# Performance work log

Measured on AMD Instinct MI355X. Metric: run time of the kernel, lower is better.

Reference implementation:

```python
import jax, jax.numpy as jnp
import numpy as np

B, S, D, U = 4, 2048, 1024, 1024

def setup_inputs() -> dict:
    key = jax.random.key(0)
    k0, k1, k2, k3 = jax.random.split(key, 4)
    scale = 1.0 / np.sqrt(D)  # keep logits sane; Glorot-like magnitude
    return {
        "inputs": jax.random.normal(k0, (B, S, D), dtype=jnp.float32),
        "W_q": jax.random.normal(k1, (D, U), dtype=jnp.float32) * scale,
        "W_k": jax.random.normal(k2, (D, U), dtype=jnp.float32) * scale,
        "W_v": jax.random.normal(k3, (D, U), dtype=jnp.float32) * scale,
    }

def reference(inputs, W_q, W_k, W_v):
    # QKV projections: [B,S,D] @ [D,U] -> [B,S,U]
    q = jnp.einsum("bsd,du->bsu", inputs, W_q)
    k = jnp.einsum("bsd,du->bsu", inputs, W_k)
    v = jnp.einsum("bsd,du->bsu", inputs, W_v)
    # Unscaled attention, as in the source (no 1/sqrt(d) factor)
    scores = jnp.einsum("bqu,bku->bqk", q, k)          # [B,S,S]
    weights = jax.nn.softmax(scores, axis=-1)
    return jnp.einsum("bqk,bku->bqu", weights, v)       # [B,S,U]
```

## Files before the change

### kernel.cpp

```cpp
#include <hip/hip_runtime.h>
#include <cstdint>
#include <cstddef>


typedef unsigned short ushort_t;
typedef _Float16 half_t;
typedef __attribute__((ext_vector_type(8))) short short8;
typedef __attribute__((ext_vector_type(4))) float floatx4;

__device__ inline unsigned short h2u(half_t h) {
  union { half_t h; unsigned short u; } v; v.h = h; return v.u;
}

__device__ __forceinline__ void gload16(const half_t* g, half_t* l) {
  __builtin_amdgcn_global_load_lds(
      (const __attribute__((address_space(1))) unsigned int*)g,
      (__attribute__((address_space(3))) unsigned int*)l, 16, 0, 0);
}

#define MX 8192
#define KCAT 2048

#define XCAT_OFF 0UL
#define WT_OFF   50331648UL
#define S_OFF    0UL
#define QCAT_OFF 69206016UL
#define KCAT_OFF 119537664UL
#define VT_OFF   169869312UL
#define WS_NEED  186646528UL

__global__ __launch_bounds__(256) void k_split_x(const float* __restrict__ X,
                                                 half_t* __restrict__ xcat) {
  long long i = (long long)blockIdx.x * 256 + threadIdx.x;
  float x = X[i];
  half_t h = (half_t)x;
  half_t lo = (half_t)(x - (float)h);
  long long row = i >> 10;
  int col = (int)(i & 1023);
  half_t* r = xcat + row * KCAT;
  r[col] = h;
  r[col + 1024] = lo;
}

__global__ __launch_bounds__(256) void k_split_wt(const float* __restrict__ Wq,
                                                  const float* __restrict__ Wk,
                                                  const float* __restrict__ Wv,
                                                  half_t* __restrict__ wt) {
  __shared__ float tile[64][65];
  const float* W = (blockIdx.z == 0) ? Wq : ((blockIdx.z == 1) ? Wk : Wv);
  half_t* out = wt + (size_t)blockIdx.z * 1024 * KCAT;
  int d0 = blockIdx.y * 64, u0 = blockIdx.x * 64;
  int t = threadIdx.x;
  int tr = t >> 6, tc = t & 63;
  for (int r = 0; r < 64; r += 4)
    tile[r + tr][tc] = W[(size_t)(d0 + r + tr) * 1024 + (u0 + tc)];
  __syncthreads();
  for (int r = 0; r < 64; r += 4) {
    int urow = r + tr, dcol = tc;
    float x = tile[dcol][urow];
    half_t h = (half_t)x;
    half_t* o = out + (size_t)(u0 + urow) * KCAT + d0;
    o[dcol] = h;
    o[dcol + 1024] = h;
  }
}

enum { EP_F32 = 0, EP_QK = 1, EP_VT = 2 };

template <int MODE>
__global__ __launch_bounds__(256, 4) void k_gemm(
    const half_t* __restrict__ A, long long aBatch, int lda,
    const half_t* __restrict__ Bt, long long bBatch, int ldb,
    void* __restrict__ Cout, long long cBatch, int ldc, int K,
    half_t* __restrict__ CoutK) {
  __shared__ __align__(16) half_t As[128 * 64];
  __shared__ __align__(16) half_t Bs[128 * 64];
  const int t = threadIdx.x;
  const int z = blockIdx.z;
  A += (long long)z * aBatch;
  Bt += (long long)z * bBatch;
  const int m0 = blockIdx.y * 128, n0 = blockIdx.x * 128;

  const int w = t >> 6, l = t & 63;
  const int lr = l & 15, quad = l >> 4;
  const int wm = (w >> 1) * 64, wn = (w & 1) * 64;

  const floatx4 fz = {0.f, 0.f, 0.f, 0.f};
  floatx4 acc[4][4];
#pragma unroll
  for (int i = 0; i < 4; i++)
#pragma unroll
    for (int j = 0; j < 4; j++) acc[i][j] = fz;

  const half_t* Ap[4];
  const half_t* Bp[4];
  half_t* ldsA[4];
  half_t* ldsB[4];
#pragma unroll
  for (int s = 0; s < 4; s++) {
    int c = s * 256 + t;
    int row = c >> 3, gq = (c & 7) ^ ((c >> 3) & 7);
    Ap[s] = A + (long long)(m0 + row) * lda + gq * 8;
    Bp[s] = Bt + (long long)(n0 + row) * ldb + gq * 8;
    ldsA[s] = &As[(s * 256 + w * 64) * 8];
    ldsB[s] = &Bs[(s * 256 + w * 64) * 8];
  }

  const int p0 = quad ^ (lr & 7);
  const int p1 = (quad + 4) ^ (lr & 7);
  const int arow = (wm + lr) * 64, brow = (wn + lr) * 64;

  for (int kb = 0; kb < K; kb += 64) {
    __syncthreads();
#pragma unroll
    for (int s = 0; s < 4; s++) {
      gload16(Ap[s] + kb, ldsA[s]);
      gload16(Bp[s] + kb, ldsB[s]);
    }
    __syncthreads();
#pragma unroll
    for (int s = 0; s < 2; s++) {
      const int pp = s ? p1 : p0;
      short8 af[4], bfg[4];
#pragma unroll
      for (int j = 0; j < 4; j++) bfg[j] = *(const short8*)&Bs[brow + j * 1024 + pp * 8];
#pragma unroll
      for (int i = 0; i < 4; i++) af[i] = *(const short8*)&As[arow + i * 1024 + pp * 8];
#pragma unroll
      for (int i = 0; i < 4; i++)
#pragma unroll
        for (int j = 0; j < 4; j++)
          acc[i][j] = __builtin_amdgcn_mfma_f32_16x16x32_f16(af[i], bfg[j], acc[i][j], 0, 0, 0);
    }
  }

#pragma unroll
  for (int i = 0; i < 4; i++) {
#pragma unroll
    for (int j = 0; j < 4; j++) {
#pragma unroll
      for (int r = 0; r < 4; r++) {
        int grow = m0 + wm + i * 16 + quad * 4 + r;
        int gcol = n0 + wn + j * 16 + lr;
        float v = acc[i][j][r];
        if (MODE == EP_F32) {
          float* C = (float*)Cout + (long long)z * cBatch;
          C[(long long)grow * ldc + gcol] = v;
        } else if (MODE == EP_QK) {
          int sel = gcol >> 10;
          int ucol = gcol & 1023;
          half_t h = (half_t)v;
          if (sel == 0) {
            half_t* pq = (half_t*)Cout + (long long)grow * KCAT;
            pq[ucol] = h;
            pq[ucol + 1024] = (half_t)(v - (float)h);
          } else {
            half_t* pk = CoutK + (long long)grow * KCAT;
            pk[ucol] = h;
            pk[ucol + 1024] = h;
          }
        } else {
          half_t* C = (half_t*)Cout;
          int b = grow >> 11, s = grow & 2047;
          C[((long long)b * 1024 + gcol) * 2048 + s] = (half_t)v;
        }
      }
    }
  }
}

__global__ __launch_bounds__(256) void k_softmax(float* __restrict__ Sbuf) {
  long long row = blockIdx.x;
  float* p = Sbuf + row * 2048;
  int t = threadIdx.x;
  float4 v0 = ((const float4*)p)[t];
  float4 v1 = ((const float4*)p)[t + 256];
  float m = fmaxf(fmaxf(fmaxf(v0.x, v0.y), fmaxf(v0.z, v0.w)),
                  fmaxf(fmaxf(v1.x, v1.y), fmaxf(v1.z, v1.w)));
  for (int off = 32; off; off >>= 1) m = fmaxf(m, __shfl_xor(m, off));
  __shared__ float red[8];
  int wv = t >> 6, ln = t & 63;
  if (ln == 0) red[wv] = m;
  __syncthreads();
  m = fmaxf(fmaxf(red[0], red[1]), fmaxf(red[2], red[3]));
  float e0 = __expf(v0.x - m), e1 = __expf(v0.y - m), e2 = __expf(v0.z - m), e3 = __expf(v0.w - m);
  float e4 = __expf(v1.x - m), e5 = __expf(v1.y - m), e6 = __expf(v1.z - m), e7 = __expf(v1.w - m);
  float s = ((e0 + e1) + (e2 + e3)) + ((e4 + e5) + (e6 + e7));
  for (int off = 32; off; off >>= 1) s += __shfl_xor(s, off);
  if (ln == 0) red[4 + wv] = s;
  __syncthreads();
  s = (red[4] + red[5]) + (red[6] + red[7]);
  float inv = 1.0f / s;
  uint2 w0, w1;
  w0.x = (unsigned)h2u((half_t)(e0 * inv)) | ((unsigned)h2u((half_t)(e1 * inv)) << 16);
  w0.y = (unsigned)h2u((half_t)(e2 * inv)) | ((unsigned)h2u((half_t)(e3 * inv)) << 16);
  w1.x = (unsigned)h2u((half_t)(e4 * inv)) | ((unsigned)h2u((half_t)(e5 * inv)) << 16);
  w1.y = (unsigned)h2u((half_t)(e6 * inv)) | ((unsigned)h2u((half_t)(e7 * inv)) << 16);
  ((uint2*)p)[t] = w0;
  ((uint2*)p)[t + 256] = w1;
}

extern "C" void kernel_launch(void* const* d_in, const int* in_sizes, int n_in,
                              void* d_out, int out_size, void* d_ws, size_t ws_size,
                              hipStream_t stream) {
  (void)in_sizes; (void)n_in; (void)out_size;
  if (ws_size < WS_NEED) return;

  const float* X = (const float*)d_in[0];
  const float* Wq = (const float*)d_in[1];
  const float* Wk = (const float*)d_in[2];
  const float* Wv = (const float*)d_in[3];
  char* ws = (char*)d_ws;
  half_t* xcat = (half_t*)(ws + XCAT_OFF);
  half_t* wt = (half_t*)(ws + WT_OFF);
  float* Sbuf = (float*)(ws + S_OFF);
  half_t* qcat = (half_t*)(ws + QCAT_OFF);
  half_t* kcat = (half_t*)(ws + KCAT_OFF);
  half_t* vt = (half_t*)(ws + VT_OFF);
  float* out = (float*)d_out;

  k_split_x<<<dim3(MX * 1024 / 256), dim3(256), 0, stream>>>(X, xcat);
  k_split_wt<<<dim3(16, 16, 3), dim3(256), 0, stream>>>(Wq, Wk, Wv, wt);

  k_gemm<EP_QK><<<dim3(16, 64, 1), dim3(256), 0, stream>>>(
      xcat, 0LL, KCAT, wt, 0LL, KCAT, qcat, 0LL, 0, KCAT, kcat);

  k_gemm<EP_VT><<<dim3(8, 64, 1), dim3(256), 0, stream>>>(
      xcat, 0LL, KCAT, wt + 2 * 1024 * KCAT, 0LL, KCAT, vt, 0LL, 0, 1024, nullptr);

  k_gemm<EP_F32><<<dim3(16, 16, 4), dim3(256), 0, stream>>>(
      qcat, (long long)2048 * KCAT, KCAT, kcat, (long long)2048 * KCAT, KCAT,
      Sbuf, (long long)2048 * 2048, 2048, KCAT, nullptr);

  k_softmax<<<dim3(8192), dim3(256), 0, stream>>>(Sbuf);

  k_gemm<EP_F32><<<dim3(8, 16, 4), dim3(256), 0, stream>>>(
      (const half_t*)Sbuf, (long long)2048 * 4096, 4096,
      vt, (long long)1024 * 2048, 2048,
      out, (long long)2048 * 1024, 1024, 2048, nullptr);
}
```

Before: 347.6 us.

## Add 256x256-tile double-buffered GEMM for QK projection and score GEMMs

Adds a new 512-thread GEMM kernel with 256x256 output tiles, a double-buffered LDS pipeline split into half-K stages, explicit vmcnt/lgkmcnt waits and raw barriers, and MFMA priority raising. It replaces the 128x128 GEMM for the fused Q/K projection and the QK^T score GEMM. The aim is to overlap global-to-LDS loads with MFMA work and to raise arithmetic intensity per tile. The cost is 128KB of LDS and heavy register use per block, and fewer blocks in flight (256 for both GEMMs).

```diff
diff --git a/kernel.cpp b/kernel.cpp
--- a/kernel.cpp
+++ b/kernel.cpp
@@ -17,6 +17,11 @@
       (const __attribute__((address_space(1))) unsigned int*)g,
       (__attribute__((address_space(3))) unsigned int*)l, 16, 0, 0);
 }
+
+#define BAR() asm volatile("s_barrier" ::: "memory")
+#define LGKM0() asm volatile("s_waitcnt lgkmcnt(0)" ::: "memory")
+#define VM6() asm volatile("s_waitcnt vmcnt(6)" ::: "memory")
+#define VM0() asm volatile("s_waitcnt vmcnt(0)" ::: "memory")
 
 #define MX 8192
 #define KCAT 2048
@@ -167,6 +172,147 @@
       }
     }
   }
+}
+
+template <int MODE>
+__global__ __launch_bounds__(512, 2) void k_gemm256(
+    const half_t* __restrict__ A, long long aBatch, int lda,
+    const half_t* __restrict__ Bt, long long bBatch, int ldb,
+    void* __restrict__ Cout, long long cBatch, int ldc, int K,
+    half_t* __restrict__ CoutK) {
+  __shared__ __align__(16) half_t As[32768];
+  __shared__ __align__(16) half_t Bs[32768];
+  const int tid = threadIdx.x;
+  const int z = blockIdx.z;
+  A += (long long)z * aBatch;
+  Bt += (long long)z * bBatch;
+  const int m0 = blockIdx.y * 256, n0 = blockIdx.x * 256;
+  const int w = tid >> 6, l = tid & 63;
+  const int lr = l & 15, quad = l >> 4;
+  const int wm = w >> 2, wn = w & 3;
+
+  const floatx4 fz = {0.f, 0.f, 0.f, 0.f};
+  floatx4 acc[8][4];
+#pragma unroll
+  for (int i = 0; i < 8; i++)
+#pragma unroll
+    for (int j = 0; j < 4; j++) acc[i][j] = fz;
+
+  const int r0 = tid >> 2;
+  const int gq0 = (tid & 3) ^ ((tid >> 3) & 3);
+  const half_t* aS0 = A + (long long)(m0 + r0) * lda + gq0 * 8;
+  const half_t* aS1 = aS0 + (long long)128 * lda;
+  const half_t* bS0 = Bt + (long long)(n0 + r0) * ldb + gq0 * 8;
+  const half_t* bS1 = bS0 + (long long)128 * ldb;
+  const int wso = w << 9;
+
+  const int swz = (quad ^ ((lr >> 1) & 3)) << 3;
+  const int aBase = wm * 4096 + lr * 32 + swz;
+  const int bBase = wn * 2048 + lr * 32 + swz;
+  const int NT = K >> 6;
+
+#define SA(BUF, KH, KOFF) do { half_t* d_ = &As[(BUF) * 16384 + (KH) * 8192 + wso]; \
+    gload16(aS0 + (KOFF), d_); gload16(aS1 + (KOFF), d_ + 4096); } while (0)
+#define SB(BUF, KH, KOFF) do { half_t* d_ = &Bs[(BUF) * 16384 + (KH) * 8192 + wso]; \
+    gload16(bS0 + (KOFF), d_); gload16(bS1 + (KOFF), d_ + 4096); } while (0)
+#define LDA4(OFF) { const half_t* ap_ = &As[(OFF)]; \
+    af0 = *(const short8*)(ap_); af1 = *(const short8*)(ap_ + 512); \
+    af2 = *(const short8*)(ap_ + 1024); af3 = *(const short8*)(ap_ + 1536); }
+#define LDB4(OFF) { const half_t* bp_ = &Bs[(OFF)]; \
+    bf0 = *(const short8*)(bp_); bf1 = *(const short8*)(bp_ + 512); \
+    bf2 = *(const short8*)(bp_ + 1024); bf3 = *(const short8*)(bp_ + 1536); }
+#define MFMA16(I0) do { \
+    acc[(I0) + 0][0] = __builtin_amdgcn_mfma_f32_16x16x32_f16(af0, bf0, acc[(I0) + 0][0], 0, 0, 0); \
+    acc[(I0) + 0][1] = __builtin_amdgcn_mfma_f32_16x16x32_f16(af0, bf1, acc[(I0) + 0][1], 0, 0, 0); \
+    acc[(I0) + 0][2] = __builtin_amdgcn_mfma_f32_16x16x32_f16(af0, bf2, acc[(I0) + 0][2], 0, 0, 0); \
+    acc[(I0) + 0][3] = __builtin_amdgcn_mfma_f32_16x16x32_f16(af0, bf3, acc[(I0) + 0][3], 0, 0, 0); \
+    acc[(I0) + 1][0] = __builtin_amdgcn_mfma_f32_16x16x32_f16(af1, bf0, acc[(I0) + 1][0], 0, 0, 0); \
+    acc[(I0) + 1][1] = __builtin_amdgcn_mfma_f32_16x16x32_f16(af1, bf1, acc[(I0) + 1][1], 0, 0, 0); \
+    acc[(I0) + 1][2] = __builtin_amdgcn_mfma_f32_16x16x32_f16(af1, bf2, acc[(I0) + 1][2], 0, 0, 0); \
+    acc[(I0) + 1][3] = __builtin_amdgcn_mfma_f32_16x16x32_f16(af1, bf3, acc[(I0) + 1][3], 0, 0, 0); \
+    acc[(I0) + 2][0] = __builtin_amdgcn_mfma_f32_16x16x32_f16(af2, bf0, acc[(I0) + 2][0], 0, 0, 0); \
+    acc[(I0) + 2][1] = __builtin_amdgcn_mfma_f32_16x16x32_f16(af2, bf1, acc[(I0) + 2][1], 0, 0, 0); \
+    acc[(I0) + 2][2] = __builtin_amdgcn_mfma_f32_16x16x32_f16(af2, bf2, acc[(I0) + 2][2], 0, 0, 0); \
+    acc[(I0) + 2][3] = __builtin_amdgcn_mfma_f32_16x16x32_f16(af2, bf3, acc[(I0) + 2][3], 0, 0, 0); \
+    acc[(I0) + 3][0] = __builtin_amdgcn_mfma_f32_16x16x32_f16(af3, bf0, acc[(I0) + 3][0], 0, 0, 0); \
+    acc[(I0) + 3][1] = __builtin_amdgcn_mfma_f32_16x16x32_f16(af3, bf1, acc[(I0) + 3][1], 0, 0, 0); \
+    acc[(I0) + 3][2] = __builtin_amdgcn_mfma_f32_16x16x32_f16(af3, bf2, acc[(I0) + 3][2], 0, 0, 0); \
+    acc[(I0) + 3][3] = __builtin_amdgcn_mfma_f32_16x16x32_f16(af3, bf3, acc[(I0) + 3][3], 0, 0, 0); \
+  } while (0)
+
+  SB(0, 0, 0); SA(0, 0, 0); SB(0, 1, 32); SA(0, 1, 32);
+  SB(1, 0, 64); SA(1, 0, 64); SB(1, 1, 96);
+  VM6();
+  BAR();
+
+  for (int t = 0; t < NT; ++t) {
+    const int buf = t & 1, nbuf = buf ^ 1;
+    const int ab = buf * 16384;
+    const int kb = t * 64;
+    short8 af0, af1, af2, af3, bf0, bf1, bf2, bf3;
+
+    LDA4(ab + aBase);
+    LDB4(ab + bBase);
+    if (t + 1 < NT) SA(nbuf, 1, kb + 96);
+    BAR(); LGKM0();
+    __builtin_amdgcn_s_setprio(1); MFMA16(0); __builtin_amdgcn_s_setprio(0);
+    BAR();
+
+    LDA4(ab + aBase + 2048);
+    if (t + 2 < NT) SB(buf, 0, kb + 128);
+    BAR(); LGKM0();
+    __builtin_amdgcn_s_setprio(1); MFMA16(4); __builtin_amdgcn_s_setprio(0);
+    BAR();
+
+    LDA4(ab + 8192 + aBase);
+    LDB4(ab + 8192 + bBase);
+    if (t + 2 < NT) SA(buf, 0, kb + 128);
+    BAR(); LGKM0();
+    __builtin_amdgcn_s_setprio(1); MFMA16(0); __builtin_amdgcn_s_setprio(0);
+    BAR();
+
+    LDA4(ab + 8192 + aBase + 2048);
+    if (t + 2 < NT) SB(buf, 1, kb + 160);
+    if (t < NT - 2) { VM6(); } else if (t == NT - 2) { VM0(); }
+    BAR(); LGKM0();
+    __builtin_amdgcn_s_setprio(1); MFMA16(4); __builtin_amdgcn_s_setprio(0);
+    BAR();
+  }
+
+#pragma unroll
+  for (int i = 0; i < 8; i++) {
+#pragma unroll
+    for (int j = 0; j < 4; j++) {
+#pragma unroll
+      for (int r = 0; r < 4; r++) {
+        int grow = m0 + wm * 128 + i * 16 + quad * 4 + r;
+        int gcol = n0 + wn * 64 + j * 16 + lr;
+        float v = acc[i][j][r];
+        if (MODE == EP_F32) {
+          float* C = (float*)Cout + (long long)z * cBatch;
+          C[(long long)grow * ldc + gcol] = v;
+        } else {
+          int sel = gcol >> 10;
+          int ucol = gcol & 1023;
+          half_t h = (half_t)v;
+          if (sel == 0) {
+            half_t* pq = (half_t*)Cout + (long long)grow * KCAT;
+            pq[ucol] = h;
+            pq[ucol + 1024] = (half_t)(v - (float)h);
+          } else {
+            half_t* pk = CoutK + (long long)grow * KCAT;
+            pk[ucol] = h;
+            pk[ucol + 1024] = h;
+          }
+        }
+      }
+    }
+  }
+#undef SA
+#undef SB
+#undef LDA4
+#undef LDB4
+#undef MFMA16
 }
 
 __global__ __launch_bounds__(256) void k_softmax(float* __restrict__ Sbuf) {
@@ -222,13 +368,13 @@
   k_split_x<<<dim3(MX * 1024 / 256), dim3(256), 0, stream>>>(X, xcat);
   k_split_wt<<<dim3(16, 16, 3), dim3(256), 0, stream>>>(Wq, Wk, Wv, wt);
 
-  k_gemm<EP_QK><<<dim3(16, 64, 1), dim3(256), 0, stream>>>(
+  k_gemm256<EP_QK><<<dim3(8, 32, 1), dim3(512), 0, stream>>>(
       xcat, 0LL, KCAT, wt, 0LL, KCAT, qcat, 0LL, 0, KCAT, kcat);
 
   k_gemm<EP_VT><<<dim3(8, 64, 1), dim3(256), 0, stream>>>(
       xcat, 0LL, KCAT, wt + 2 * 1024 * KCAT, 0LL, KCAT, vt, 0LL, 0, 1024, nullptr);
 
-  k_gemm<EP_F32><<<dim3(16, 16, 4), dim3(256), 0, stream>>>(
+  k_gemm256<EP_F32><<<dim3(8, 8, 4), dim3(512), 0, stream>>>(
       qcat, (long long)2048 * KCAT, KCAT, kcat, (long long)2048 * KCAT, KCAT,
       Sbuf, (long long)2048 * 2048, 2048, KCAT, nullptr);
 
```

New measurement: 336.7 us. 3.1% less time.
